# Optimization experiments

Measured on AMD Instinct MI355X. Metric: run time of the kernel, lower is better.

## Reference

```python
import jax, jax.numpy as jnp
import numpy as np

N = 200000
E = 6400000
G = 2048
HID = 32
EPS = 1e-5


def setup_inputs() -> dict:
    key = jax.random.key(0)
    ks = jax.random.split(key, 12)
    x = jax.random.normal(ks[0], (N, 1), dtype=jnp.float32)
    edge_index = jax.random.randint(ks[1], (2, E), 0, N, dtype=jnp.int64)
    batch = jnp.sort(jax.random.randint(ks[2], (N,), 0, G, dtype=jnp.int64))
    s1 = 1.0  # fan_in=1
    s2 = 1.0 / np.sqrt(HID)
    return {
        "x": x,
        "edge_index": edge_index,
        "batch": batch,
        # SAGEConv1: lin_l (neighbors, with bias) and lin_r (root, no bias)
        "W1l": jax.random.normal(ks[3], (HID, 1), jnp.float32) * s1,
        "b1l": jnp.zeros((HID,), jnp.float32),
        "W1r": jax.random.normal(ks[4], (HID, 1), jnp.float32) * s1,
        # SAGEConv2
        "W2l": jax.random.normal(ks[5], (HID, HID), jnp.float32) * s2,
        "b2l": jnp.zeros((HID,), jnp.float32),
        "W2r": jax.random.normal(ks[6], (HID, HID), jnp.float32) * s2,
        # BatchNorms (affine)
        "g1": jnp.ones((HID,), jnp.float32),
        "be1": jnp.zeros((HID,), jnp.float32),
        "g2": jnp.ones((HID,), jnp.float32),
        "be2": jnp.zeros((HID,), jnp.float32),
        # attention gate Linear(hidden, 1)
        "gate_w": jax.random.normal(ks[7], (1, HID), jnp.float32) * s2,
        "gate_b": jnp.zeros((1,), jnp.float32),
        # final Linear(hidden, 1)
        "lin_w": jax.random.normal(ks[8], (1, HID), jnp.float32) * s2,
        "lin_b": jnp.zeros((1,), jnp.float32),
    }


def _sage(x, src, dst, Wl, bl, Wr):
    # mean aggregation of neighbor messages x_j = x[src] at dst
    msg = x[src]                                              # [E, F]
    agg = jax.ops.segment_sum(msg, dst, num_segments=N)       # [N, F]
    deg = jax.ops.segment_sum(jnp.ones((src.shape[0], 1), x.dtype), dst, num_segments=N)
    agg = agg / jnp.maximum(deg, 1.0)
    return agg @ Wl.T + bl + x @ Wr.T


def _bn(x, gamma, beta):
    mu = jnp.mean(x, axis=0)
    var = jnp.mean((x - mu) ** 2, axis=0)  # biased variance, as torch BN
    return (x - mu) * jax.lax.rsqrt(var + EPS) * gamma + beta


def reference(x, edge_index, batch, W1l, b1l, W1r, W2l, b2l, W2r,
              g1, be1, g2, be2, gate_w, gate_b, lin_w, lin_b):
    src, dst = edge_index[0], edge_index[1]
    h = jax.nn.relu(_bn(_sage(x, src, dst, W1l, b1l, W1r), g1, be1))
    h = jax.nn.relu(_bn(_sage(h, src, dst, W2l, b2l, W2r), g2, be2))
    # attentional aggregation: segment softmax over gate scores
    score = (h @ gate_w.T + gate_b)                           # [N, 1]
    smax = jax.ops.segment_max(score, batch, num_segments=G)  # [G, 1]
    ex = jnp.exp(score - smax[batch])
    denom = jax.ops.segment_sum(ex, batch, num_segments=G)    # [G, 1]
    alpha = ex / denom[batch]
    g = jax.ops.segment_sum(alpha * h, batch, num_segments=G) # [G, HID]
    return jax.nn.sigmoid((g @ lin_w.T + lin_b)[:, 0])
```

## Files before the change

kernel.cpp:

```cpp
#include <hip/hip_runtime.h>
#include <math.h>

#define N_NODES 200000
#define N_EDGES 6400000
#define N_GRAPHS 2048
#define HID 32
#define BN_EPS 1e-5f

#define NPB 256
#define NBUCK ((N_NODES + NPB - 1) / NPB)
#define CAP 8960
#define PART_CHUNK 8192
#define NPARTBLK ((N_EDGES + PART_CHUNK - 1) / PART_CHUNK)

#define NPC 64
#define NBLK_C (N_NODES / NPC)

#define RED_BLKS 64
#define RED_CHUNK ((NBLK_C + RED_BLKS - 1) / RED_BLKS)

__device__ inline float relu_f(float v) { return fmaxf(v, 0.f); }

__global__ void k_init(int* __restrict__ cursor) {
    int t = blockIdx.x * blockDim.x + threadIdx.x;
    if (t < NBUCK) cursor[t] = t * CAP;
}

__launch_bounds__(256)
__global__ void k_part(const int* __restrict__ src, const int* __restrict__ dst,
                       int* __restrict__ cursor, unsigned int* __restrict__ ebuf) {
    __shared__ int histL[NBUCK];
    __shared__ int baseL[NBUCK];
    int tid = threadIdx.x;
    for (int i = tid; i < NBUCK; i += 256) histL[i] = 0;
    __syncthreads();
    int e0 = blockIdx.x * PART_CHUNK;
    int e1 = min(e0 + PART_CHUNK, N_EDGES);
    int4 dreg[8];
#pragma unroll
    for (int i = 0; i < 8; i++) {
        int base = e0 + (i * 256 + tid) * 4;
        if (base < e1) {
            int4 d4 = *(const int4*)(dst + base);
            dreg[i] = d4;
            atomicAdd(&histL[d4.x >> 8], 1);
            atomicAdd(&histL[d4.y >> 8], 1);
            atomicAdd(&histL[d4.z >> 8], 1);
            atomicAdd(&histL[d4.w >> 8], 1);
        } else {
            dreg[i] = make_int4(-1, -1, -1, -1);
        }
    }
    __syncthreads();
    for (int i = tid; i < NBUCK; i += 256) {
        int c = histL[i];
        if (c) baseL[i] = atomicAdd(&cursor[i], c);
        histL[i] = 0;
    }
    __syncthreads();
#pragma unroll
    for (int i = 0; i < 8; i++) {
        int base = e0 + (i * 256 + tid) * 4;
        if (base < e1) {
            int4 s4 = *(const int4*)(src + base);
            int4 d4 = dreg[i];
            int b, r, pos;
            b = d4.x >> 8; r = atomicAdd(&histL[b], 1); pos = baseL[b] + r;
            if (pos < (b + 1) * CAP) ebuf[pos] = (unsigned)(s4.x & 0x3FFFF) | ((unsigned)(d4.x & 255) << 18);
            b = d4.y >> 8; r = atomicAdd(&histL[b], 1); pos = baseL[b] + r;
            if (pos < (b + 1) * CAP) ebuf[pos] = (unsigned)(s4.y & 0x3FFFF) | ((unsigned)(d4.y & 255) << 18);
            b = d4.z >> 8; r = atomicAdd(&histL[b], 1); pos = baseL[b] + r;
            if (pos < (b + 1) * CAP) ebuf[pos] = (unsigned)(s4.z & 0x3FFFF) | ((unsigned)(d4.z & 255) << 18);
            b = d4.w >> 8; r = atomicAdd(&histL[b], 1); pos = baseL[b] + r;
            if (pos < (b + 1) * CAP) ebuf[pos] = (unsigned)(s4.w & 0x3FFFF) | ((unsigned)(d4.w & 255) << 18);
        }
    }
}

__launch_bounds__(256)
__global__ void k_sort(const unsigned int* __restrict__ ebuf, const int* __restrict__ cursor,
                       const float* __restrict__ x, int* __restrict__ ebuf2,
                       int* __restrict__ deg, int* __restrict__ offs,
                       float* __restrict__ ax, float* __restrict__ part1) {
    __shared__ int degL[NPB], scanL[NPB], offL[NPB], cntL[NPB];
    __shared__ float red[4][5];
    int tid = threadIdx.x;
    degL[tid] = 0;
    cntL[tid] = 0;
    __syncthreads();
    int b = blockIdx.x;
    int p0 = b * CAP;
    int cnt = min(cursor[b] - p0, CAP);
    for (int i = tid; i < cnt; i += 256)
        atomicAdd(&degL[ebuf[p0 + i] >> 18], 1);
    __syncthreads();
    int d = degL[tid];
    scanL[tid] = d;
    __syncthreads();
    for (int off = 1; off < NPB; off <<= 1) {
        int y = (tid >= off) ? scanL[tid - off] : 0;
        __syncthreads();
        scanL[tid] += y;
        __syncthreads();
    }
    int myoff = scanL[tid] - d;
    offL[tid] = myoff;
    __syncthreads();
    int node = b * NPB + tid;
    if (node < N_NODES) { deg[node] = d; offs[node] = p0 + myoff; }
    for (int i = tid; i < cnt; i += 256) {
        unsigned v = ebuf[p0 + i];
        int ld = v >> 18;
        int r = atomicAdd(&cntL[ld], 1);
        ebuf2[p0 + offL[ld] + r] = (int)(v & 0x3FFFF);
    }
    __syncthreads();
    float sum = 0.f;
    int base = p0 + myoff;
    int j = 0;
    for (; j + 8 <= d; j += 8) {
        int ss[8];
#pragma unroll
        for (int k = 0; k < 8; k++) ss[k] = ebuf2[base + j + k];
        float acc = 0.f;
#pragma unroll
        for (int k = 0; k < 8; k++) acc += x[ss[k]];
        sum += acc;
    }
    for (; j < d; j++) sum += x[ebuf2[base + j]];
    float an = 0.f, xn = 0.f;
    if (node < N_NODES) {
        an = sum / (float)max(d, 1);
        xn = x[node];
        ax[2 * node] = an;
        ax[2 * node + 1] = xn;
    }
    float sa = an, sx = xn, saa = an * an, sxx = xn * xn, sax = an * xn;
    for (int o = 32; o; o >>= 1) {
        sa += __shfl_down(sa, o);
        sx += __shfl_down(sx, o);
        saa += __shfl_down(saa, o);
        sxx += __shfl_down(sxx, o);
        sax += __shfl_down(sax, o);
    }
    int w = tid >> 6;
    if ((tid & 63) == 0) {
        red[w][0] = sa; red[w][1] = sx; red[w][2] = saa; red[w][3] = sxx; red[w][4] = sax;
    }
    __syncthreads();
    if (tid < 5)
        part1[b * 8 + tid] = red[0][tid] + red[1][tid] + red[2][tid] + red[3][tid];
}

__launch_bounds__(256)
__global__ void k_params1(const float* __restrict__ part1,
                          const float* __restrict__ W1l, const float* __restrict__ b1l,
                          const float* __restrict__ W1r, const float* __restrict__ g1,
                          const float* __restrict__ be1, float* __restrict__ pABC) {
    int tid = threadIdx.x;
    double loc[5] = {0, 0, 0, 0, 0};
    for (int b = tid; b < NBUCK; b += 256) {
#pragma unroll
        for (int s = 0; s < 5; s++) loc[s] += (double)part1[b * 8 + s];
    }
    for (int o = 32; o; o >>= 1) {
#pragma unroll
        for (int s = 0; s < 5; s++) loc[s] += __shfl_down(loc[s], o);
    }
    __shared__ double red[4][5];
    __shared__ double st[5];
    int w = tid >> 6;
    if ((tid & 63) == 0) {
#pragma unroll
        for (int s = 0; s < 5; s++) red[w][s] = loc[s];
    }
    __syncthreads();
    if (tid < 5) st[tid] = red[0][tid] + red[1][tid] + red[2][tid] + red[3][tid];
    __syncthreads();
    int f = tid;
    if (f < HID) {
        double invN = 1.0 / (double)N_NODES;
        double ma = st[0] * invN, mx = st[1] * invN;
        double va = st[2] * invN - ma * ma;
        double vx = st[3] * invN - mx * mx;
        double cax = st[4] * invN - ma * mx;
        double wl = (double)W1l[f], wr = (double)W1r[f];
        double mu = wl * ma + wr * mx + (double)b1l[f];
        double var = wl * wl * va + wr * wr * vx + 2.0 * wl * wr * cax;
        double s = (double)g1[f] / sqrt(var + (double)BN_EPS);
        pABC[f] = (float)(wl * s);
        pABC[HID + f] = (float)(wr * s);
        pABC[2 * HID + f] = (float)(((double)b1l[f] - mu) * s + (double)be1[f]);
    }
}

__launch_bounds__(256)
__global__ void k_conv2(const int* __restrict__ ebuf2, const int* __restrict__ offs,
                        const int* __restrict__ deg, const float* __restrict__ ax,
                        const float* __restrict__ pABC,
                        const float* __restrict__ W2l, const float* __restrict__ W2r,
                        const float* __restrict__ b2l, float* __restrict__ h2pre,
                        float* __restrict__ part2) {
    __shared__ float aggL[NPC * (HID + 1)];
    __shared__ __align__(16) float2 pairL[8 * 32];
    __shared__ float A_s[HID], B_s[HID], C_s[HID];
    int tid = threadIdx.x;
    if (tid < HID) {
        A_s[tid] = pABC[tid];
        B_s[tid] = pABC[HID + tid];
        C_s[tid] = pABC[2 * HID + tid];
    }
    __syncthreads();
    int b = blockIdx.x;
    int f = tid & 31;
    int grp = tid >> 5;
    float Af = A_s[f], Bf = B_s[f], Cf = C_s[f];
    const float2* ax2 = (const float2*)ax;
    float2* myStage = pairL + grp * 32;
    const float4* myStage4 = (const float4*)myStage;
#pragma unroll 1
    for (int i = 0; i < NPC / 8; i++) {
        int ln = i * 8 + grp;
        int node = b * NPC + ln;
        int dg = deg[node], off = offs[node];
        float m = 0.f;
#pragma unroll 1
        for (int j = 0; j < dg; j += 32) {
            int rem = min(32, dg - j);
            float2 pv = make_float2(0.f, 0.f);
            if (f < rem) pv = ax2[ebuf2[off + j + f]];
            myStage[f] = pv;
            int k = 0;
            for (; k + 2 <= rem; k += 2) {
                float4 q = myStage4[k >> 1];
                m += relu_f(fmaf(q.x, Af, fmaf(q.y, Bf, Cf)));
                m += relu_f(fmaf(q.z, Af, fmaf(q.w, Bf, Cf)));
            }
            if (k < rem) {
                float2 q = myStage[k];
                m += relu_f(fmaf(q.x, Af, fmaf(q.y, Bf, Cf)));
            }
        }
        aggL[ln * (HID + 1) + f] = m / (float)max(dg, 1);
    }
    __syncthreads();
    int nl = tid & 63;
    int fg = tid >> 6;
    int node = b * NPC + nl;
    float2 axn = ax2[node];
    float an = axn.x, xn = axn.y;
    float ag[HID], h1[HID];
#pragma unroll
    for (int k = 0; k < HID; k++) {
        ag[k] = aggL[nl * (HID + 1) + k];
        h1[k] = relu_f(fmaf(an, A_s[k], fmaf(xn, B_s[k], C_s[k])));
    }
    float v[8];
#pragma unroll
    for (int lf = 0; lf < 8; lf++) {
        int ff = fg * 8 + lf;
        const float4* wl4 = (const float4*)(W2l + ff * HID);
        const float4* wr4 = (const float4*)(W2r + ff * HID);
        float s = b2l[ff];
#pragma unroll
        for (int q = 0; q < HID / 4; q++) {
            float4 wl = wl4[q], wr = wr4[q];
            s = fmaf(ag[4 * q],     wl.x, fmaf(h1[4 * q],     wr.x, s));
            s = fmaf(ag[4 * q + 1], wl.y, fmaf(h1[4 * q + 1], wr.y, s));
            s = fmaf(ag[4 * q + 2], wl.z, fmaf(h1[4 * q + 2], wr.z, s));
            s = fmaf(ag[4 * q + 3], wl.w, fmaf(h1[4 * q + 3], wr.w, s));
        }
        v[lf] = s;
    }
    float4* op = (float4*)(h2pre + (size_t)node * HID + fg * 8);
    op[0] = make_float4(v[0], v[1], v[2], v[3]);
    op[1] = make_float4(v[4], v[5], v[6], v[7]);
#pragma unroll
    for (int lf = 0; lf < 8; lf++) {
        float s1v = v[lf], s2v = v[lf] * v[lf];
        for (int o = 32; o; o >>= 1) {
            s1v += __shfl_down(s1v, o);
            s2v += __shfl_down(s2v, o);
        }
        if (nl == 0) {
            part2[(size_t)b * 64 + fg * 8 + lf] = s1v;
            part2[(size_t)b * 64 + 32 + fg * 8 + lf] = s2v;
        }
    }
}

__launch_bounds__(256)
__global__ void k_red2(const float* __restrict__ part2, double* __restrict__ mid) {
    __shared__ double st2[4][64];
    int tid = threadIdx.x;
    int q = tid >> 6, t = tid & 63;
    int b0 = blockIdx.x * RED_CHUNK;
    int b1 = min(b0 + RED_CHUNK, NBLK_C);
    double s = 0.0;
    for (int b = b0 + q; b < b1; b += 4) s += (double)part2[(size_t)b * 64 + t];
    st2[q][t] = s;
    __syncthreads();
    if (tid < 64)
        mid[(size_t)blockIdx.x * 64 + tid] = st2[0][tid] + st2[1][tid] + st2[2][tid] + st2[3][tid];
}

__launch_bounds__(256)
__global__ void k_params2(const double* __restrict__ mid, const float* __restrict__ g2,
                          const float* __restrict__ be2, float* __restrict__ pPQ) {
    __shared__ double st2[4][64];
    __shared__ double st[64];
    int tid = threadIdx.x;
    int q = tid >> 6, t = tid & 63;
    double s = 0.0;
    for (int i = q; i < RED_BLKS; i += 4) s += mid[(size_t)i * 64 + t];
    st2[q][t] = s;
    __syncthreads();
    if (tid < 64) st[tid] = st2[0][tid] + st2[1][tid] + st2[2][tid] + st2[3][tid];
    __syncthreads();
    if (tid < HID) {
        double invN = 1.0 / (double)N_NODES;
        double mu = st[tid] * invN;
        double var = st[HID + tid] * invN - mu * mu;
        double sc = (double)g2[tid] / sqrt(var + (double)BN_EPS);
        pPQ[tid] = (float)sc;
        pPQ[HID + tid] = (float)((double)be2[tid] - mu * sc);
    }
}

#define FIN_TPB 128
__launch_bounds__(FIN_TPB)
__global__ void k_final(const float* __restrict__ h2pre, const int* __restrict__ batch,
                        const float* __restrict__ pPQ, const float* __restrict__ gate_w,
                        const float* __restrict__ gate_b, const float* __restrict__ lin_w,
                        const float* __restrict__ lin_b, float* __restrict__ out) {
    __shared__ int sh_lo, sh_hi;
    __shared__ float red[2][HID + 2];
    __shared__ float sh_P[HID], sh_Q[HID], sh_gw[HID], sh_lw[HID];
    int g = blockIdx.x;
    if (threadIdx.x == 0) {
        int lo = 0, hi = N_NODES;
        while (lo < hi) { int mid = (lo + hi) >> 1; if (batch[mid] < g) lo = mid + 1; else hi = mid; }
        sh_lo = lo;
        int lo2 = lo, hi2 = N_NODES;
        int key2 = g + 1;
        while (lo2 < hi2) { int mid = (lo2 + hi2) >> 1; if (batch[mid] < key2) lo2 = mid + 1; else hi2 = mid; }
        sh_hi = lo2;
    }
    if (threadIdx.x < HID) {
        sh_P[threadIdx.x] = pPQ[threadIdx.x];
        sh_Q[threadIdx.x] = pPQ[HID + threadIdx.x];
        sh_gw[threadIdx.x] = gate_w[threadIdx.x];
        sh_lw[threadIdx.x] = lin_w[threadIdx.x];
    }
    __syncthreads();
    int lo = sh_lo, hi = sh_hi;
    float gb = gate_b[0];

    float mx = -3.0e38f;
    for (int n = lo + threadIdx.x; n < hi; n += FIN_TPB) {
        const float4* hp = (const float4*)(h2pre + (size_t)n * HID);
        float sc = gb;
#pragma unroll
        for (int i = 0; i < HID / 4; i++) {
            float4 v = hp[i];
            sc += relu_f(fmaf(v.x, sh_P[4 * i], sh_Q[4 * i])) * sh_gw[4 * i];
            sc += relu_f(fmaf(v.y, sh_P[4 * i + 1], sh_Q[4 * i + 1])) * sh_gw[4 * i + 1];
            sc += relu_f(fmaf(v.z, sh_P[4 * i + 2], sh_Q[4 * i + 2])) * sh_gw[4 * i + 2];
            sc += relu_f(fmaf(v.w, sh_P[4 * i + 3], sh_Q[4 * i + 3])) * sh_gw[4 * i + 3];
        }
        mx = fmaxf(mx, sc);
    }
    for (int o = 32; o; o >>= 1) mx = fmaxf(mx, __shfl_down(mx, o));
    if ((threadIdx.x & 63) == 0) red[threadIdx.x >> 6][0] = mx;
    __syncthreads();
    float smax = fmaxf(red[0][0], red[1][0]);
    __syncthreads();

    float S = 0.f;
    float T[HID];
#pragma unroll
    for (int f = 0; f < HID; f++) T[f] = 0.f;
    for (int n = lo + threadIdx.x; n < hi; n += FIN_TPB) {
        const float4* hp = (const float4*)(h2pre + (size_t)n * HID);
        float h[HID];
        float sc = gb;
#pragma unroll
        for (int i = 0; i < HID / 4; i++) {
            float4 v = hp[i];
            h[4 * i]     = relu_f(fmaf(v.x, sh_P[4 * i],     sh_Q[4 * i]));
            h[4 * i + 1] = relu_f(fmaf(v.y, sh_P[4 * i + 1], sh_Q[4 * i + 1]));
            h[4 * i + 2] = relu_f(fmaf(v.z, sh_P[4 * i + 2], sh_Q[4 * i + 2]));
            h[4 * i + 3] = relu_f(fmaf(v.w, sh_P[4 * i + 3], sh_Q[4 * i + 3]));
            sc += h[4 * i] * sh_gw[4 * i] + h[4 * i + 1] * sh_gw[4 * i + 1]
                + h[4 * i + 2] * sh_gw[4 * i + 2] + h[4 * i + 3] * sh_gw[4 * i + 3];
        }
        float e = __expf(sc - smax);
        S += e;
#pragma unroll
        for (int f = 0; f < HID; f++) T[f] += e * h[f];
    }
    for (int o = 32; o; o >>= 1) {
        S += __shfl_down(S, o);
#pragma unroll
        for (int f = 0; f < HID; f++) T[f] += __shfl_down(T[f], o);
    }
    if ((threadIdx.x & 63) == 0) {
        int w = threadIdx.x >> 6;
        red[w][1] = S;
#pragma unroll
        for (int f = 0; f < HID; f++) red[w][2 + f] = T[f];
    }
    __syncthreads();
    if (threadIdx.x == 0) {
        float St = red[0][1] + red[1][1];
        float z = lin_b[0];
        if (St > 0.f) {
            float inv = 1.f / St;
#pragma unroll
            for (int f = 0; f < HID; f++)
                z += (red[0][2 + f] + red[1][2 + f]) * inv * sh_lw[f];
        }
        out[g] = 1.f / (1.f + __expf(-z));
    }
}

extern "C" void kernel_launch(void* const* d_in, const int* in_sizes, int n_in,
                              void* d_out, int out_size, void* d_ws, size_t ws_size,
                              hipStream_t stream) {
    const float* x = (const float*)d_in[0];
    const int* ei = (const int*)d_in[1];
    const int* batch = (const int*)d_in[2];
    const float* W1l = (const float*)d_in[3];
    const float* b1l = (const float*)d_in[4];
    const float* W1r = (const float*)d_in[5];
    const float* W2l = (const float*)d_in[6];
    const float* b2l = (const float*)d_in[7];
    const float* W2r = (const float*)d_in[8];
    const float* g1 = (const float*)d_in[9];
    const float* be1 = (const float*)d_in[10];
    const float* g2 = (const float*)d_in[11];
    const float* be2 = (const float*)d_in[12];
    const float* gate_w = (const float*)d_in[13];
    const float* gate_b = (const float*)d_in[14];
    const float* lin_w = (const float*)d_in[15];
    const float* lin_b = (const float*)d_in[16];

    const int* srcp = ei;
    const int* dstp = ei + N_EDGES;

    char* ws = (char*)d_ws;
    size_t p = 0;
    auto alloc = [&](size_t bytes) -> char* {
        char* r = ws + p;
        p = (p + bytes + 255) & ~(size_t)255;
        return r;
    };
    unsigned int* ebuf = (unsigned int*)alloc((size_t)NBUCK * CAP * 4);
    int* ebuf2 = (int*)alloc((size_t)NBUCK * CAP * 4);
    float* ax = (float*)alloc((size_t)N_NODES * 2 * 4);
    int* deg = (int*)alloc((size_t)N_NODES * 4);
    int* offs = (int*)alloc((size_t)N_NODES * 4);
    int* cursor = (int*)alloc((size_t)NBUCK * 4);
    float* pABC = (float*)alloc(96 * 4);
    float* pPQ = (float*)alloc(64 * 4);
    float* part1 = (float*)alloc((size_t)NBUCK * 8 * 4);
    float* part2 = (float*)alloc((size_t)NBLK_C * 64 * 4);
    double* mid = (double*)alloc((size_t)RED_BLKS * 64 * 8);
    float* h2pre = (float*)ebuf;

    k_init<<<1, 1024, 0, stream>>>(cursor);
    k_part<<<NPARTBLK, 256, 0, stream>>>(srcp, dstp, cursor, ebuf);
    k_sort<<<NBUCK, 256, 0, stream>>>(ebuf, cursor, x, ebuf2, deg, offs, ax, part1);
    k_params1<<<1, 256, 0, stream>>>(part1, W1l, b1l, W1r, g1, be1, pABC);
    k_conv2<<<NBLK_C, 256, 0, stream>>>(ebuf2, offs, deg, ax, pABC, W2l, W2r, b2l, h2pre, part2);
    k_red2<<<RED_BLKS, 256, 0, stream>>>(part2, mid);
    k_params2<<<1, 256, 0, stream>>>(mid, g2, be2, pPQ);
    k_final<<<N_GRAPHS, FIN_TPB, 0, stream>>>(h2pre, batch, pPQ, gate_w, gate_b, lin_w, lin_b,
                                              (float*)d_out);
}
```

Baseline: 511.2 us.

## Reuse histogram atomic ranks in partitioning and prefetch neighbor gathers in conv2

The partition and sort kernels now keep the rank returned by the first shared-memory atomic histogram pass in registers and reuse it as the scatter offset. This removes the second round of shared atomics and the counter reset. The conv2 aggregation loop is flattened into a single software-pipelined loop that loads the next 32-edge chunk's gathered features while the current chunk is reduced, with degree and offset values staged in shared memory. The trade-off is higher register pressure (35-entry rank array in k_sort, rank int4s in k_part), which could lower occupancy.

```diff
diff --git a/kernel.cpp b/kernel.cpp
--- a/kernel.cpp
+++ b/kernel.cpp
@@ -37,16 +37,17 @@
     int e0 = blockIdx.x * PART_CHUNK;
     int e1 = min(e0 + PART_CHUNK, N_EDGES);
     int4 dreg[8];
+    int4 rreg[8];
 #pragma unroll
     for (int i = 0; i < 8; i++) {
         int base = e0 + (i * 256 + tid) * 4;
         if (base < e1) {
             int4 d4 = *(const int4*)(dst + base);
             dreg[i] = d4;
-            atomicAdd(&histL[d4.x >> 8], 1);
-            atomicAdd(&histL[d4.y >> 8], 1);
-            atomicAdd(&histL[d4.z >> 8], 1);
-            atomicAdd(&histL[d4.w >> 8], 1);
+            rreg[i].x = atomicAdd(&histL[d4.x >> 8], 1);
+            rreg[i].y = atomicAdd(&histL[d4.y >> 8], 1);
+            rreg[i].z = atomicAdd(&histL[d4.z >> 8], 1);
+            rreg[i].w = atomicAdd(&histL[d4.w >> 8], 1);
         } else {
             dreg[i] = make_int4(-1, -1, -1, -1);
         }
@@ -55,7 +56,6 @@
     for (int i = tid; i < NBUCK; i += 256) {
         int c = histL[i];
         if (c) baseL[i] = atomicAdd(&cursor[i], c);
-        histL[i] = 0;
     }
     __syncthreads();
 #pragma unroll
@@ -64,14 +64,15 @@
         if (base < e1) {
             int4 s4 = *(const int4*)(src + base);
             int4 d4 = dreg[i];
-            int b, r, pos;
-            b = d4.x >> 8; r = atomicAdd(&histL[b], 1); pos = baseL[b] + r;
+            int4 r4 = rreg[i];
+            int b, pos;
+            b = d4.x >> 8; pos = baseL[b] + r4.x;
             if (pos < (b + 1) * CAP) ebuf[pos] = (unsigned)(s4.x & 0x3FFFF) | ((unsigned)(d4.x & 255) << 18);
-            b = d4.y >> 8; r = atomicAdd(&histL[b], 1); pos = baseL[b] + r;
+            b = d4.y >> 8; pos = baseL[b] + r4.y;
             if (pos < (b + 1) * CAP) ebuf[pos] = (unsigned)(s4.y & 0x3FFFF) | ((unsigned)(d4.y & 255) << 18);
-            b = d4.z >> 8; r = atomicAdd(&histL[b], 1); pos = baseL[b] + r;
+            b = d4.z >> 8; pos = baseL[b] + r4.z;
             if (pos < (b + 1) * CAP) ebuf[pos] = (unsigned)(s4.z & 0x3FFFF) | ((unsigned)(d4.z & 255) << 18);
-            b = d4.w >> 8; r = atomicAdd(&histL[b], 1); pos = baseL[b] + r;
+            b = d4.w >> 8; pos = baseL[b] + r4.w;
             if (pos < (b + 1) * CAP) ebuf[pos] = (unsigned)(s4.w & 0x3FFFF) | ((unsigned)(d4.w & 255) << 18);
         }
     }
@@ -82,17 +83,20 @@
                        const float* __restrict__ x, int* __restrict__ ebuf2,
                        int* __restrict__ deg, int* __restrict__ offs,
                        float* __restrict__ ax, float* __restrict__ part1) {
-    __shared__ int degL[NPB], scanL[NPB], offL[NPB], cntL[NPB];
+    __shared__ int degL[NPB], scanL[NPB], offL[NPB];
     __shared__ float red[4][5];
     int tid = threadIdx.x;
     degL[tid] = 0;
-    cntL[tid] = 0;
     __syncthreads();
     int b = blockIdx.x;
     int p0 = b * CAP;
     int cnt = min(cursor[b] - p0, CAP);
-    for (int i = tid; i < cnt; i += 256)
-        atomicAdd(&degL[ebuf[p0 + i] >> 18], 1);
+    int rk[35];
+#pragma unroll
+    for (int it = 0; it < 35; it++) {
+        int i = tid + it * 256;
+        if (i < cnt) rk[it] = atomicAdd(&degL[ebuf[p0 + i] >> 18], 1);
+    }
     __syncthreads();
     int d = degL[tid];
     scanL[tid] = d;
@@ -108,11 +112,14 @@
     __syncthreads();
     int node = b * NPB + tid;
     if (node < N_NODES) { deg[node] = d; offs[node] = p0 + myoff; }
-    for (int i = tid; i < cnt; i += 256) {
-        unsigned v = ebuf[p0 + i];
-        int ld = v >> 18;
-        int r = atomicAdd(&cntL[ld], 1);
-        ebuf2[p0 + offL[ld] + r] = (int)(v & 0x3FFFF);
+#pragma unroll
+    for (int it = 0; it < 35; it++) {
+        int i = tid + it * 256;
+        if (i < cnt) {
+            unsigned v = ebuf[p0 + i];
+            int ld = v >> 18;
+            ebuf2[p0 + offL[ld] + rk[it]] = (int)(v & 0x3FFFF);
+        }
     }
     __syncthreads();
     float sum = 0.f;
@@ -204,44 +211,62 @@
     __shared__ float aggL[NPC * (HID + 1)];
     __shared__ __align__(16) float2 pairL[8 * 32];
     __shared__ float A_s[HID], B_s[HID], C_s[HID];
+    __shared__ int degS[NPC], offS[NPC];
     int tid = threadIdx.x;
+    int b = blockIdx.x;
     if (tid < HID) {
         A_s[tid] = pABC[tid];
         B_s[tid] = pABC[HID + tid];
         C_s[tid] = pABC[2 * HID + tid];
     }
-    __syncthreads();
-    int b = blockIdx.x;
+    if (tid < NPC) {
+        degS[tid] = deg[b * NPC + tid];
+        offS[tid] = offs[b * NPC + tid];
+    }
+    __syncthreads();
     int f = tid & 31;
     int grp = tid >> 5;
     float Af = A_s[f], Bf = B_s[f], Cf = C_s[f];
     const float2* ax2 = (const float2*)ax;
     float2* myStage = pairL + grp * 32;
     const float4* myStage4 = (const float4*)myStage;
+    float m = 0.f;
+    int iC = 0, jC = 0;
+    float2 pvP = make_float2(0.f, 0.f);
+    {
+        int rem0 = min(32, degS[grp]);
+        if (f < rem0) pvP = ax2[ebuf2[offS[grp] + f]];
+    }
 #pragma unroll 1
-    for (int i = 0; i < NPC / 8; i++) {
-        int ln = i * 8 + grp;
-        int node = b * NPC + ln;
-        int dg = deg[node], off = offs[node];
-        float m = 0.f;
-#pragma unroll 1
-        for (int j = 0; j < dg; j += 32) {
-            int rem = min(32, dg - j);
-            float2 pv = make_float2(0.f, 0.f);
-            if (f < rem) pv = ax2[ebuf2[off + j + f]];
-            myStage[f] = pv;
-            int k = 0;
-            for (; k + 2 <= rem; k += 2) {
-                float4 q = myStage4[k >> 1];
-                m += relu_f(fmaf(q.x, Af, fmaf(q.y, Bf, Cf)));
-                m += relu_f(fmaf(q.z, Af, fmaf(q.w, Bf, Cf)));
-            }
-            if (k < rem) {
-                float2 q = myStage[k];
-                m += relu_f(fmaf(q.x, Af, fmaf(q.y, Bf, Cf)));
-            }
-        }
-        aggL[ln * (HID + 1) + f] = m / (float)max(dg, 1);
+    while (iC < 8) {
+        int dgC = degS[iC * 8 + grp];
+        int iN = iC, jN = jC + 32;
+        if (jN >= dgC) { iN = iC + 1; jN = 0; }
+        float2 pvN = make_float2(0.f, 0.f);
+        if (iN < 8) {
+            int slotN = iN * 8 + grp;
+            int remN = min(32, degS[slotN] - jN);
+            if (f < remN) pvN = ax2[ebuf2[offS[slotN] + jN + f]];
+        }
+        int rem = min(32, dgC - jC);
+        myStage[f] = pvP;
+        int k = 0;
+        for (; k + 2 <= rem; k += 2) {
+            float4 q = myStage4[k >> 1];
+            m += relu_f(fmaf(q.x, Af, fmaf(q.y, Bf, Cf)));
+            m += relu_f(fmaf(q.z, Af, fmaf(q.w, Bf, Cf)));
+        }
+        if (k < rem) {
+            float2 q = myStage[k];
+            m += relu_f(fmaf(q.x, Af, fmaf(q.y, Bf, Cf)));
+        }
+        if (iN != iC) {
+            int ln = iC * 8 + grp;
+            aggL[ln * (HID + 1) + f] = m / (float)max(dgC, 1);
+            m = 0.f;
+        }
+        iC = iN; jC = jN;
+        pvP = pvN;
     }
     __syncthreads();
     int nl = tid & 63;
```

After: 513.9 us. Within noise of the previous version (+0.5%).
